# Kernel tuning notes

Hardware: AMD Instinct MI355X
Metric: run time of the kernel (lower is better)

## Reference

```python
import jax, jax.numpy as jnp
import numpy as np


def setup_inputs() -> dict:
    key = jax.random.key(0)
    k_adj, k_ann, k_b = jax.random.split(key, 3)
    B, N, F = 8, 4096, 64
    # Adjacency: sparse-ish nonnegative matrix (TF version stores it as tf.sparse;
    raw = jax.random.uniform(k_adj, (B, N, N), dtype=jnp.float32)
    adjacent = jnp.where(raw > 0.95, raw, 0.0)
    annotations = jax.random.normal(k_ann, (B, N, F), dtype=jnp.float32)
    bias = jax.random.normal(k_b, (1, 1, F), dtype=jnp.float32)
    return {"adjacent": adjacent, "annotations": annotations, "bias": bias}


def reference(adjacent, annotations, bias):
    # Per-batch sparse @ dense matmul in TF == batched matmul here.
    # adjacent: [B,N,N], annotations: [B,N,F] -> [B,N,F]
    out = jnp.einsum('bnm,bmf->bnf', adjacent, annotations)
    return out + bias
```

## Files before the change

kernel.cpp:

```cpp
#include <hip/hip_runtime.h>
#include <stdint.h>

typedef __bf16 bf16x8 __attribute__((ext_vector_type(8)));
typedef float f32x16 __attribute__((ext_vector_type(16)));

#define NN 4096
#define FF 64

__device__ __forceinline__ unsigned short f2bf(float x) {
    unsigned int u = __builtin_bit_cast(unsigned int, x);
    unsigned int r = u + 0x7fffu + ((u >> 16) & 1u);
    return (unsigned short)(r >> 16);
}

__device__ __forceinline__ unsigned int pk2(float lo, float hi) {
    return (unsigned int)f2bf(lo) | ((unsigned int)f2bf(hi) << 16);
}

__global__ __launch_bounds__(256) void annT_kernel(const float* __restrict__ ann,
                                                   unsigned short* __restrict__ annT) {
    __shared__ unsigned short tile[FF * 66];
    int b = blockIdx.x >> 6;
    int m0 = (blockIdx.x & 63) << 6;
    int t = threadIdx.x;
    int f = t & 63;
    int ml = t >> 6;
    const float* src = ann + ((size_t)(b * NN + m0)) * FF;
#pragma unroll
    for (int it = 0; it < 16; ++it) {
        int m = it * 4 + ml;
        tile[f * 66 + m] = f2bf(src[(size_t)m * FF + f]);
    }
    __syncthreads();
    int m2 = (t & 31) * 2;
    int fr = t >> 5;
    unsigned short* dst = annT + (size_t)b * FF * NN + m0;
#pragma unroll
    for (int it = 0; it < 8; ++it) {
        int fo = it * 8 + fr;
        unsigned int lo = tile[fo * 66 + m2];
        unsigned int hi = tile[fo * 66 + m2 + 1];
        *(unsigned int*)(dst + (size_t)fo * NN + m2) = lo | (hi << 16);
    }
}

__global__ __launch_bounds__(64) void gconv_kernel(const float* __restrict__ A,
                                                   const unsigned short* __restrict__ annT,
                                                   const float* __restrict__ bias,
                                                   float* __restrict__ out) {
    int bi = blockIdx.x;
    int b = bi & 7;
    int n0 = (bi >> 3) << 5;
    int lane = threadIdx.x;
    int r = lane & 31;
    int h = lane >> 5;

    const float* Ap = A + (size_t)b * NN * NN + (size_t)(n0 + r) * NN + h * 8;
    const unsigned short* B0p = annT + (size_t)b * FF * NN + (size_t)r * NN + h * 8;
    const unsigned short* B1p = B0p + (size_t)32 * NN;

    f32x16 acc0 = {}, acc1 = {};

    float4 aA[4][2]; uint4 bA0[4], bA1[4];
    float4 aB[4][2]; uint4 bB0[4], bB1[4];

    auto loadSet = [&](float4 (&a)[4][2], uint4 (&b0)[4], uint4 (&b1)[4], int k0) {
#pragma unroll
        for (int j = 0; j < 4; ++j) {
            int k = k0 + j * 16;
            a[j][0] = *(const float4*)(Ap + k);
            a[j][1] = *(const float4*)(Ap + k + 4);
            b0[j] = *(const uint4*)(B0p + k);
            b1[j] = *(const uint4*)(B1p + k);
        }
    };
    auto compSet = [&](float4 (&a)[4][2], uint4 (&b0)[4], uint4 (&b1)[4]) {
#pragma unroll
        for (int j = 0; j < 4; ++j) {
            uint4 ap;
            ap.x = pk2(a[j][0].x, a[j][0].y);
            ap.y = pk2(a[j][0].z, a[j][0].w);
            ap.z = pk2(a[j][1].x, a[j][1].y);
            ap.w = pk2(a[j][1].z, a[j][1].w);
            bf16x8 af = __builtin_bit_cast(bf16x8, ap);
            acc0 = __builtin_amdgcn_mfma_f32_32x32x16_bf16(
                af, __builtin_bit_cast(bf16x8, b0[j]), acc0, 0, 0, 0);
            acc1 = __builtin_amdgcn_mfma_f32_32x32x16_bf16(
                af, __builtin_bit_cast(bf16x8, b1[j]), acc1, 0, 0, 0);
        }
    };

    loadSet(aA, bA0, bA1, 0);
#pragma unroll 1
    for (int k0 = 0; k0 < NN; k0 += 128) {
        loadSet(aB, bB0, bB1, k0 + 64);
        compSet(aA, bA0, bA1);
        if (k0 + 128 < NN) loadSet(aA, bA0, bA1, k0 + 128);
        compSet(aB, bB0, bB1);
    }

    float bv0 = bias[r], bv1 = bias[32 + r];
    float* ob = out + ((size_t)(b * NN + n0)) * FF;
#pragma unroll
    for (int t = 0; t < 16; ++t) {
        int rowl = (t & 3) + 8 * (t >> 2) + h * 4;
        ob[(size_t)rowl * FF + r] = acc0[t] + bv0;
        ob[(size_t)rowl * FF + 32 + r] = acc1[t] + bv1;
    }
}

extern "C" void kernel_launch(void* const* d_in, const int* in_sizes, int n_in,
                              void* d_out, int out_size, void* d_ws, size_t ws_size,
                              hipStream_t stream) {
    const float* adj = (const float*)d_in[0];
    const float* ann = (const float*)d_in[1];
    const float* bias = (const float*)d_in[2];
    float* out = (float*)d_out;
    unsigned short* annT = (unsigned short*)d_ws;

    annT_kernel<<<dim3(8 * (NN / 64)), dim3(256), 0, stream>>>(ann, annT);
    gconv_kernel<<<dim3(8 * (NN / 32)), dim3(64), 0, stream>>>(adj, annT, bias, out);
}
```

Measured before the change: 729.2 us.

## Stage A and annT tiles through swizzled LDS with direct global-to-LDS loads

Replaces the single-wave, register-prefetch matmul with a 4-wave block that computes a 64-row tile. A and transposed annotations are loaded straight into XOR-swizzled LDS with global_load_lds and double-buffered across K steps, separated by barriers. The aim is to share the annT tile across waves, raise memory-level parallelism and use fewer registers while the fp32 A stream stays bandwidth-bound. In exchange it adds barrier synchronisation per K step and halves the grid size.

Measured after the change: 707.3 us. 1.03x faster.

```diff
diff --git a/kernel.cpp b/kernel.cpp
--- a/kernel.cpp
+++ b/kernel.cpp
@@ -6,6 +6,9 @@
 
 #define NN 4096
 #define FF 64
+#define BM 64
+#define BK 64
+#define NSTEP (NN / BK)
 
 __device__ __forceinline__ unsigned short f2bf(float x) {
     unsigned int u = __builtin_bit_cast(unsigned int, x);
@@ -13,8 +16,9 @@
     return (unsigned short)(r >> 16);
 }
 
-__device__ __forceinline__ unsigned int pk2(float lo, float hi) {
-    return (unsigned int)f2bf(lo) | ((unsigned int)f2bf(hi) << 16);
+__device__ __forceinline__ void gload16(const void* g, void* l) {
+    __builtin_amdgcn_global_load_lds((const __attribute__((address_space(1))) void*)g,
+                                     (__attribute__((address_space(3))) void*)l, 16, 0, 0);
 }
 
 __global__ __launch_bounds__(256) void annT_kernel(const float* __restrict__ ann,
@@ -44,68 +48,95 @@
     }
 }
 
-__global__ __launch_bounds__(64) void gconv_kernel(const float* __restrict__ A,
-                                                   const unsigned short* __restrict__ annT,
-                                                   const float* __restrict__ bias,
-                                                   float* __restrict__ out) {
+__global__ __launch_bounds__(256, 2) void gconv_kernel(const float* __restrict__ A,
+                                                       const unsigned short* __restrict__ annT,
+                                                       const float* __restrict__ bias,
+                                                       float* __restrict__ out) {
+    __shared__ alignas(16) char lds[2][24576];
+
     int bi = blockIdx.x;
     int b = bi & 7;
-    int n0 = (bi >> 3) << 5;
-    int lane = threadIdx.x;
-    int r = lane & 31;
-    int h = lane >> 5;
+    int n0 = (bi >> 3) << 6;
+    int t = threadIdx.x, lane = t & 63, wid = t >> 6;
+    int wm = wid >> 1, wf = wid & 1;
+    int r = lane & 31, h = lane >> 5;
 
-    const float* Ap = A + (size_t)b * NN * NN + (size_t)(n0 + r) * NN + h * 8;
-    const unsigned short* B0p = annT + (size_t)b * FF * NN + (size_t)r * NN + h * 8;
-    const unsigned short* B1p = B0p + (size_t)32 * NN;
+    const float* Ab = A + (size_t)b * NN * NN + (size_t)n0 * NN;
+    const unsigned short* Tb = annT + (size_t)b * FF * NN;
 
-    f32x16 acc0 = {}, acc1 = {};
+    const float* asrc[4];
+#pragma unroll
+    for (int j = 0; j < 4; ++j) {
+        unsigned s = (unsigned)(wid * 4096 + j * 1024 + lane * 16);
+        unsigned row = s >> 8;
+        unsigned q = ((s & 255u) ^ ((row & 15u) << 4)) >> 4;
+        asrc[j] = Ab + (size_t)row * NN + q * 4;
+    }
+    const unsigned short* bsrc[2];
+#pragma unroll
+    for (int j = 0; j < 2; ++j) {
+        unsigned s = (unsigned)(wid * 2048 + j * 1024 + lane * 16);
+        unsigned f = s >> 7;
+        unsigned q = ((s & 127u) ^ ((f & 7u) << 4)) >> 4;
+        bsrc[j] = Tb + (size_t)f * NN + q * 8;
+    }
 
-    float4 aA[4][2]; uint4 bA0[4], bA1[4];
-    float4 aB[4][2]; uint4 bB0[4], bB1[4];
-
-    auto loadSet = [&](float4 (&a)[4][2], uint4 (&b0)[4], uint4 (&b1)[4], int k0) {
+    auto STAGE = [&](int buf, int k0) {
+        char* base = lds[buf];
 #pragma unroll
-        for (int j = 0; j < 4; ++j) {
-            int k = k0 + j * 16;
-            a[j][0] = *(const float4*)(Ap + k);
-            a[j][1] = *(const float4*)(Ap + k + 4);
-            b0[j] = *(const uint4*)(B0p + k);
-            b1[j] = *(const uint4*)(B1p + k);
-        }
-    };
-    auto compSet = [&](float4 (&a)[4][2], uint4 (&b0)[4], uint4 (&b1)[4]) {
+        for (int j = 0; j < 4; ++j)
+            gload16(asrc[j] + k0, base + wid * 4096 + j * 1024);
 #pragma unroll
-        for (int j = 0; j < 4; ++j) {
-            uint4 ap;
-            ap.x = pk2(a[j][0].x, a[j][0].y);
-            ap.y = pk2(a[j][0].z, a[j][0].w);
-            ap.z = pk2(a[j][1].x, a[j][1].y);
-            ap.w = pk2(a[j][1].z, a[j][1].w);
-            bf16x8 af = __builtin_bit_cast(bf16x8, ap);
-            acc0 = __builtin_amdgcn_mfma_f32_32x32x16_bf16(
-                af, __builtin_bit_cast(bf16x8, b0[j]), acc0, 0, 0, 0);
-            acc1 = __builtin_amdgcn_mfma_f32_32x32x16_bf16(
-                af, __builtin_bit_cast(bf16x8, b1[j]), acc1, 0, 0, 0);
-        }
+        for (int j = 0; j < 2; ++j)
+            gload16(bsrc[j] + k0, base + 16384 + wid * 2048 + j * 1024);
     };
 
-    loadSet(aA, bA0, bA1, 0);
+    int arow = wm * 32 + r;
+    unsigned abase = (unsigned)(arow * 256);
+    unsigned aswz = (unsigned)((arow & 15) << 4);
+    int frow = wf * 32 + r;
+    unsigned bbase = (unsigned)(frow * 128);
+    unsigned bswz = (unsigned)((frow & 7) << 4);
+
+    f32x16 acc = {};
+
+    STAGE(0, 0);
 #pragma unroll 1
-    for (int k0 = 0; k0 < NN; k0 += 128) {
-        loadSet(aB, bB0, bB1, k0 + 64);
-        compSet(aA, bA0, bA1);
-        if (k0 + 128 < NN) loadSet(aA, bA0, bA1, k0 + 128);
-        compSet(aB, bB0, bB1);
+    for (int s = 0; s < NSTEP; ++s) {
+        int cur = s & 1;
+        if (s + 1 < NSTEP) {
+            STAGE(cur ^ 1, (s + 1) * BK);
+            asm volatile("s_waitcnt vmcnt(6)" ::: "memory");
+        } else {
+            asm volatile("s_waitcnt vmcnt(0)" ::: "memory");
+        }
+        __builtin_amdgcn_s_barrier();
+        asm volatile("" ::: "memory");
+
+        const char* bufA = lds[cur];
+        const char* bufB = lds[cur] + 16384;
+#pragma unroll
+        for (int kc = 0; kc < 4; ++kc) {
+            unsigned ao = abase + (unsigned)(kc * 64 + h * 32);
+            float4 a0 = *(const float4*)(bufA + ((ao) ^ aswz));
+            float4 a1 = *(const float4*)(bufA + ((ao + 16) ^ aswz));
+            bf16x8 af = {(__bf16)a0.x, (__bf16)a0.y, (__bf16)a0.z, (__bf16)a0.w,
+                         (__bf16)a1.x, (__bf16)a1.y, (__bf16)a1.z, (__bf16)a1.w};
+            unsigned bo = (bbase + (unsigned)(kc * 32 + h * 16)) ^ bswz;
+            bf16x8 bf = *(const bf16x8*)(bufB + bo);
+            acc = __builtin_amdgcn_mfma_f32_32x32x16_bf16(af, bf, acc, 0, 0, 0);
+        }
+        asm volatile("" ::: "memory");
+        __builtin_amdgcn_s_barrier();
+        asm volatile("" ::: "memory");
     }
 
-    float bv0 = bias[r], bv1 = bias[32 + r];
-    float* ob = out + ((size_t)(b * NN + n0)) * FF;
+    float bv = bias[wf * 32 + r];
+    float* ob = out + ((size_t)(b * NN + n0 + wm * 32)) * FF + wf * 32 + r;
 #pragma unroll
-    for (int t = 0; t < 16; ++t) {
-        int rowl = (t & 3) + 8 * (t >> 2) + h * 4;
-        ob[(size_t)rowl * FF + r] = acc0[t] + bv0;
-        ob[(size_t)rowl * FF + 32 + r] = acc1[t] + bv1;
+    for (int e = 0; e < 16; ++e) {
+        int rowl = (e & 3) + 8 * (e >> 2) + h * 4;
+        ob[(size_t)rowl * FF] = acc[e] + bv;
     }
 }
 
@@ -119,5 +150,5 @@
     unsigned short* annT = (unsigned short*)d_ws;
 
     annT_kernel<<<dim3(8 * (NN / 64)), dim3(256), 0, stream>>>(ann, annT);
-    gconv_kernel<<<dim3(8 * (NN / 32)), dim3(64), 0, stream>>>(adj, annT, bias, out);
+    gconv_kernel<<<dim3(8 * (NN / BM)), dim3(256), 0, stream>>>(adj, annT, bias, out);
 }
```
